# Performance work log

Hardware: AMD Instinct MI355X
Metric: run time of the kernel (lower is better)

The kernel has to match this reference:

```python
import jax, jax.numpy as jnp
import numpy as np

PATCH_W = 5  # from init_kwargs


def _fold(x, H, W, k):
    # x: (N, C*k*k, L) with L = (H-k+1)*(W-k+1), stride=1 col2im scatter-add
    N, CKK, L = x.shape
    oh, ow = H - k + 1, W - k + 1
    C = CKK // (k * k)
    x = x.reshape(N, C, k, k, oh, ow)
    out = jnp.zeros((N, C, H, W), x.dtype)
    for di in range(k):
        for dj in range(k):
            out = out.at[:, :, di:di + oh, dj:dj + ow].add(x[:, :, di, dj])
    return out


def _unfold(img, k):
    # img: (N, C, H, W) -> (N, C*k*k, L), stride=1 im2col gather
    N, C, H, W = img.shape
    oh, ow = H - k + 1, W - k + 1
    cols = jnp.stack(
        [img[:, :, di:di + oh, dj:dj + ow] for di in range(k) for dj in range(k)],
        axis=2,
    )  # (N, C, k*k, oh, ow)
    return cols.reshape(N, C * k * k, oh * ow)


def setup_inputs() -> dict:
    key = jax.random.key(0)
    images, hor_f, ver_f = 8, 64, 25
    pixels_h = pixels_w = 64
    patches = (pixels_h - PATCH_W + 1) * (pixels_w - PATCH_W + 1)  # 3600
    x = jax.random.normal(key, (images, patches, hor_f, ver_f), dtype=jnp.float32)
    return {"x": x, "pixels_h": pixels_h, "pixels_w": pixels_w}


def reference(x, pixels_h, pixels_w):
    k = PATCH_W
    images, patches, hor_f, ver_f = x.shape
    # (images, patches, hor_f, ver_f) -> (images*hor_f, ver_f, patches)
    xc = jnp.transpose(x, (0, 2, 3, 1)).reshape(images * hor_f, ver_f, patches)
    # overlap count per output pixel (fold of ones)
    ones = jnp.ones((1, ver_f, patches), xc.dtype)
    patch_cnt = _fold(ones, pixels_h, pixels_w, k)  # (1, C, H, W)
    img = _fold(xc, pixels_h, pixels_w, k) / patch_cnt
    cols = _unfold(img, k)  # (images*hor_f, ver_f, patches)
    out = cols.reshape(images, hor_f, ver_f, patches)
    return jnp.transpose(out, (0, 3, 1, 2))
```

## Files before the change

### kernel.cpp

```cpp
#include <hip/hip_runtime.h>

#define OH     60
#define NIMG   8
#define HF     64
#define VF     25
#define NPATCH 3600
#define CDIM   1600

typedef float floatx4 __attribute__((ext_vector_type(4)));

#define FH   8
#define FC   (FH * VF)
#define SPI  5
#define PJS  64
#define NSTRIP 12
#define SROWS  9

__global__ __launch_bounds__(512, 6) void fold_kernel(const float* __restrict__ x,
                                                      float* __restrict__ slab) {
    __shared__ float lb[FC * PJS];
    const int b = blockIdx.x;
    const int im = b & 7;
    const int rem = b >> 3;
    const int hg = rem & 7, strip = rem >> 3;
    const int t = threadIdx.x;
    const int h0 = hg * FH;
    const int pi0 = strip * SPI;
    const int j = t & 63, g = t >> 6;

    float acc[SROWS];
#pragma unroll
    for (int k = 0; k < SROWS; ++k) acc[k] = 0.f;

    const float* xb = x + ((size_t)im * NPATCH + (size_t)pi0 * OH) * CDIM + h0 * VF;

    int off_g[6], off_l[6];
#pragma unroll
    for (int k = 0; k < 6; ++k) {
        int u = t + 512 * k;
        if (u < 3000) {
            int pj = u / 50, c4 = u - 50 * pj;
            off_g[k] = pj * CDIM + (c4 << 2);
            off_l[k] = (c4 << 8) + (pj ^ (c4 & 31));
        }
    }

    float4 stg[6];
#pragma unroll
    for (int k = 0; k < 6; ++k)
        if (t + 512 * k < 3000)
            stg[k] = *reinterpret_cast<const float4*>(xb + off_g[k]);

#pragma unroll
    for (int row = 0; row < SPI; ++row) {
        if (row) __syncthreads();
#pragma unroll
        for (int k = 0; k < 6; ++k)
            if (t + 512 * k < 3000) {
                float4 v = stg[k];
                int a = off_l[k];
                lb[a]           = v.x;
                lb[a + PJS]     = v.y;
                lb[a + 2 * PJS] = v.z;
                lb[a + 3 * PJS] = v.w;
            }
        if (row + 1 < SPI) {
#pragma unroll
            for (int k = 0; k < 6; ++k)
                if (t + 512 * k < 3000)
                    stg[k] = *reinterpret_cast<const float4*>(
                        xb + (size_t)(row + 1) * OH * CDIM + off_g[k]);
        }
        __syncthreads();
#pragma unroll
        for (int di = 0; di < 5; ++di) {
#pragma unroll
            for (int dj = 0; dj < 5; ++dj) {
                int c = g * VF + di * 5 + dj;
                int pjr = j - dj;
                if ((unsigned)pjr < 60u)
                    acc[row + di] += lb[c * PJS + (pjr ^ ((c >> 2) & 31))];
            }
        }
    }

    float* sb = slab + (((size_t)(strip * 8 + im) * 64 + h0 + g) * SROWS) * 64 + j;
#pragma unroll
    for (int il = 0; il < SROWS; ++il) sb[il * 64] = acc[il];
}

#define UH   16
#define LJS  68

__global__ __launch_bounds__(256) void unfold_kernel(const float* __restrict__ slab,
                                                     float* __restrict__ out) {
    __shared__ float li[UH * 5 * LJS];
    __shared__ int4 lut[100];
    const int b = blockIdx.x;
    const int im = b & 7;
    const int rem = b >> 3;
    const int hh = rem & 3, pi = rem >> 2;
    const int t = threadIdx.x;
    const int h0 = hh * UH;

    if (t < 100) {
        int4 e;
        int* ep = &e.x;
#pragma unroll
        for (int k = 0; k < 4; ++k) {
            int fl = 4 * t + k;
            int ho = fl / 25, v = fl - 25 * ho;
            int di = v / 5, dj = v - 5 * di;
            ep[k] = (ho * 5 + di) * LJS + dj;
        }
        lut[t] = e;
    }

    for (int u = t; u < UH * 5 * 16; u += 256) {
        int ch = u / 80, rem2 = u - 80 * ch;
        int di = rem2 >> 4, j4 = rem2 & 15;
        int i = pi + di;
        int s_hi = min(i / 5, NSTRIP - 1);
        int s_lo = (i <= 8) ? 0 : (i - 4) / 5;
        const float* pa = slab +
            (((size_t)(s_lo * 8 + im) * 64 + h0 + ch) * SROWS + (i - 5 * s_lo)) * 64 + (j4 << 2);
        float4 v = *reinterpret_cast<const float4*>(pa);
        if (s_hi != s_lo) {
            const float* pb = slab +
                (((size_t)(s_hi * 8 + im) * 64 + h0 + ch) * SROWS + (i - 5 * s_hi)) * 64 + (j4 << 2);
            float4 w = *reinterpret_cast<const float4*>(pb);
            v.x += w.x; v.y += w.y; v.z += w.z; v.w += w.w;
        }
        float ri = 1.0f / (float)min(min(i + 1, 64 - i), 5);
        int jb = j4 << 2;
        float4 w;
        w.x = v.x * ri * (1.0f / (float)min(min(jb + 1, 64 - jb), 5));
        w.y = v.y * ri * (1.0f / (float)min(min(jb + 2, 63 - jb), 5));
        w.z = v.z * ri * (1.0f / (float)min(min(jb + 3, 62 - jb), 5));
        w.w = v.w * ri * (1.0f / (float)min(min(jb + 4, 61 - jb), 5));
        *reinterpret_cast<float4*>(&li[(ch * 5 + di) * LJS + jb]) = w;
    }
    __syncthreads();

    float* ob = out + ((size_t)im * NPATCH + (size_t)pi * OH) * CDIM + h0 * VF;
    for (int u = t; u < 6000; u += 256) {
        int pj = u / 100, r = u - 100 * pj;
        int4 e = lut[r];
        floatx4 o;
        o.x = li[e.x + pj];
        o.y = li[e.y + pj];
        o.z = li[e.z + pj];
        o.w = li[e.w + pj];
        __builtin_nontemporal_store(o,
            reinterpret_cast<floatx4*>(ob + (size_t)pj * CDIM + 4 * r));
    }
}

extern "C" void kernel_launch(void* const* d_in, const int* in_sizes, int n_in,
                              void* d_out, int out_size, void* d_ws, size_t ws_size,
                              hipStream_t stream) {
    const float* x = (const float*)d_in[0];
    float* slab = (float*)d_ws;
    float* out  = (float*)d_out;

    fold_kernel<<<768, 512, 0, stream>>>(x, slab);
    unfold_kernel<<<1920, 256, 0, stream>>>(slab, out);

    (void)out_size; (void)ws_size; (void)in_sizes; (void)n_in;
}
```

Before: 76.31 us.

## Fuse fold and unfold into one sliding-window kernel with halo recompute

```diff
diff --git a/kernel.cpp b/kernel.cpp
--- a/kernel.cpp
+++ b/kernel.cpp
@@ -9,30 +9,34 @@
 
 typedef float floatx4 __attribute__((ext_vector_type(4)));
 
-#define FH   8
-#define FC   (FH * VF)
-#define SPI  5
-#define PJS  64
-#define NSTRIP 12
-#define SROWS  9
+#define FH    8
+#define FC    200
+#define PJS   64
+#define SPP   15
+#define NACC  19
+#define JP2   65
+#define ROWSZ (8 * JP2)
 
-__global__ __launch_bounds__(512, 6) void fold_kernel(const float* __restrict__ x,
-                                                      float* __restrict__ slab) {
+__global__ __launch_bounds__(512) void fused_kernel(const float* __restrict__ x,
+                                                    float* __restrict__ out) {
     __shared__ float lb[FC * PJS];
+    __shared__ float li2[6 * ROWSZ];
     const int b = blockIdx.x;
     const int im = b & 7;
     const int rem = b >> 3;
     const int hg = rem & 7, strip = rem >> 3;
     const int t = threadIdx.x;
     const int h0 = hg * FH;
-    const int pi0 = strip * SPI;
+    const int pi0 = strip * SPP;
     const int j = t & 63, g = t >> 6;
 
-    float acc[SROWS];
+    const float rcj = 1.0f / (float)min(min(j + 1, 64 - j), 5);
+
+    float acc[NACC];
 #pragma unroll
-    for (int k = 0; k < SROWS; ++k) acc[k] = 0.f;
+    for (int k = 0; k < NACC; ++k) acc[k] = 0.f;
 
-    const float* xb = x + ((size_t)im * NPATCH + (size_t)pi0 * OH) * CDIM + h0 * VF;
+    const float* xb = x + (size_t)im * NPATCH * CDIM + h0 * VF;
 
     int off_g[6], off_l[6];
 #pragma unroll
@@ -45,114 +49,109 @@
         }
     }
 
+    int outoff[6], colb[6][4], dic[6][4];
+#pragma unroll
+    for (int k = 0; k < 6; ++k) {
+        int u = t + 512 * k;
+        if (u < 3000) {
+            int pj = u / 50, s = u - 50 * pj;
+            outoff[k] = pj * CDIM + (s << 2);
+#pragma unroll
+            for (int c = 0; c < 4; ++c) {
+                int fl = (s << 2) + c;
+                int ho = fl / 25, v = fl - 25 * ho;
+                int di = v / 5, dj = v - 5 * di;
+                colb[k][c] = ho * JP2 + pj + dj;
+                dic[k][c] = di;
+            }
+        }
+    }
+
     float4 stg[6];
-#pragma unroll
-    for (int k = 0; k < 6; ++k)
-        if (t + 512 * k < 3000)
-            stg[k] = *reinterpret_cast<const float4*>(xb + off_g[k]);
-
-#pragma unroll
-    for (int row = 0; row < SPI; ++row) {
-        if (row) __syncthreads();
-#pragma unroll
-        for (int k = 0; k < 6; ++k)
-            if (t + 512 * k < 3000) {
-                float4 v = stg[k];
-                int a = off_l[k];
-                lb[a]           = v.x;
-                lb[a + PJS]     = v.y;
-                lb[a + 2 * PJS] = v.z;
-                lb[a + 3 * PJS] = v.w;
-            }
-        if (row + 1 < SPI) {
+    {
+        int rho = pi0 - 4;
+        if (rho >= 0) {
 #pragma unroll
             for (int k = 0; k < 6; ++k)
                 if (t + 512 * k < 3000)
                     stg[k] = *reinterpret_cast<const float4*>(
-                        xb + (size_t)(row + 1) * OH * CDIM + off_g[k]);
-        }
-        __syncthreads();
-#pragma unroll
-        for (int di = 0; di < 5; ++di) {
-#pragma unroll
-            for (int dj = 0; dj < 5; ++dj) {
-                int c = g * VF + di * 5 + dj;
-                int pjr = j - dj;
-                if ((unsigned)pjr < 60u)
-                    acc[row + di] += lb[c * PJS + (pjr ^ ((c >> 2) & 31))];
-            }
+                        xb + (size_t)rho * OH * CDIM + off_g[k]);
         }
     }
 
-    float* sb = slab + (((size_t)(strip * 8 + im) * 64 + h0 + g) * SROWS) * 64 + j;
 #pragma unroll
-    for (int il = 0; il < SROWS; ++il) sb[il * 64] = acc[il];
-}
+    for (int r = 0; r < 24; ++r) {
+        const int rho = pi0 - 4 + r;
+        const bool sv = (r <= 22) && (rho >= 0) && (rho <= 59);
 
-#define UH   16
-#define LJS  68
+        if (sv) {
+#pragma unroll
+            for (int k = 0; k < 6; ++k)
+                if (t + 512 * k < 3000) {
+                    float4 v = stg[k];
+                    int a = off_l[k];
+                    lb[a]           = v.x;
+                    lb[a + PJS]     = v.y;
+                    lb[a + 2 * PJS] = v.z;
+                    lb[a + 3 * PJS] = v.w;
+                }
+        }
+        if (r >= 9) {
+            float* op = out + ((size_t)im * NPATCH + (size_t)(pi0 + r - 9) * OH) * CDIM
+                            + h0 * VF;
+            const int base = (r - 9) % 6;
+#pragma unroll
+            for (int k = 0; k < 6; ++k)
+                if (t + 512 * k < 3000) {
+                    floatx4 o;
+                    { int sl = base + dic[k][0]; sl -= (sl >= 6) ? 6 : 0;
+                      o.x = li2[sl * ROWSZ + colb[k][0]]; }
+                    { int sl = base + dic[k][1]; sl -= (sl >= 6) ? 6 : 0;
+                      o.y = li2[sl * ROWSZ + colb[k][1]]; }
+                    { int sl = base + dic[k][2]; sl -= (sl >= 6) ? 6 : 0;
+                      o.z = li2[sl * ROWSZ + colb[k][2]]; }
+                    { int sl = base + dic[k][3]; sl -= (sl >= 6) ? 6 : 0;
+                      o.w = li2[sl * ROWSZ + colb[k][3]]; }
+                    __builtin_nontemporal_store(o,
+                        reinterpret_cast<floatx4*>(op + outoff[k]));
+                }
+        }
+        __syncthreads();
 
-__global__ __launch_bounds__(256) void unfold_kernel(const float* __restrict__ slab,
-                                                     float* __restrict__ out) {
-    __shared__ float li[UH * 5 * LJS];
-    __shared__ int4 lut[100];
-    const int b = blockIdx.x;
-    const int im = b & 7;
-    const int rem = b >> 3;
-    const int hh = rem & 3, pi = rem >> 2;
-    const int t = threadIdx.x;
-    const int h0 = hh * UH;
-
-    if (t < 100) {
-        int4 e;
-        int* ep = &e.x;
+        if (sv) {
 #pragma unroll
-        for (int k = 0; k < 4; ++k) {
-            int fl = 4 * t + k;
-            int ho = fl / 25, v = fl - 25 * ho;
-            int di = v / 5, dj = v - 5 * di;
-            ep[k] = (ho * 5 + di) * LJS + dj;
+            for (int di = 0; di < 5; ++di) {
+                const int il = r - 4 + di;
+                if (il >= 0 && il < NACC) {
+#pragma unroll
+                    for (int dj = 0; dj < 5; ++dj) {
+                        int c = g * VF + di * 5 + dj;
+                        int pjr = j - dj;
+                        if ((unsigned)pjr < 60u)
+                            acc[il] += lb[c * PJS + (pjr ^ ((c >> 2) & 31))];
+                    }
+                }
+            }
         }
-        lut[t] = e;
-    }
-
-    for (int u = t; u < UH * 5 * 16; u += 256) {
-        int ch = u / 80, rem2 = u - 80 * ch;
-        int di = rem2 >> 4, j4 = rem2 & 15;
-        int i = pi + di;
-        int s_hi = min(i / 5, NSTRIP - 1);
-        int s_lo = (i <= 8) ? 0 : (i - 4) / 5;
-        const float* pa = slab +
-            (((size_t)(s_lo * 8 + im) * 64 + h0 + ch) * SROWS + (i - 5 * s_lo)) * 64 + (j4 << 2);
-        float4 v = *reinterpret_cast<const float4*>(pa);
-        if (s_hi != s_lo) {
-            const float* pb = slab +
-                (((size_t)(s_hi * 8 + im) * 64 + h0 + ch) * SROWS + (i - 5 * s_hi)) * 64 + (j4 << 2);
-            float4 w = *reinterpret_cast<const float4*>(pb);
-            v.x += w.x; v.y += w.y; v.z += w.z; v.w += w.w;
+        if (r < 23) {
+            int rho2 = rho + 1;
+            if (r + 1 <= 22 && rho2 >= 0 && rho2 <= 59) {
+#pragma unroll
+                for (int k = 0; k < 6; ++k)
+                    if (t + 512 * k < 3000)
+                        stg[k] = *reinterpret_cast<const float4*>(
+                            xb + (size_t)rho2 * OH * CDIM + off_g[k]);
+            }
         }
-        float ri = 1.0f / (float)min(min(i + 1, 64 - i), 5);
-        int jb = j4 << 2;
-        float4 w;
-        w.x = v.x * ri * (1.0f / (float)min(min(jb + 1, 64 - jb), 5));
-        w.y = v.y * ri * (1.0f / (float)min(min(jb + 2, 63 - jb), 5));
-        w.z = v.z * ri * (1.0f / (float)min(min(jb + 3, 62 - jb), 5));
-        w.w = v.w * ri * (1.0f / (float)min(min(jb + 4, 61 - jb), 5));
-        *reinterpret_cast<float4*>(&li[(ch * 5 + di) * LJS + jb]) = w;
-    }
-    __syncthreads();
-
-    float* ob = out + ((size_t)im * NPATCH + (size_t)pi * OH) * CDIM + h0 * VF;
-    for (int u = t; u < 6000; u += 256) {
-        int pj = u / 100, r = u - 100 * pj;
-        int4 e = lut[r];
-        floatx4 o;
-        o.x = li[e.x + pj];
-        o.y = li[e.y + pj];
-        o.z = li[e.z + pj];
-        o.w = li[e.w + pj];
-        __builtin_nontemporal_store(o,
-            reinterpret_cast<floatx4*>(ob + (size_t)pj * CDIM + 4 * r));
+        if (r >= 4 && r <= 22) {
+            const int il = r - 4;
+            const int i = pi0 + il;
+            float ri = 0.2f;
+            if (i < 4) ri = 1.0f / (float)(i + 1);
+            else if (i > 59) ri = 1.0f / (float)(64 - i);
+            li2[(il % 6) * ROWSZ + g * JP2 + j] = acc[il] * ri * rcj;
+        }
+        __syncthreads();
     }
 }
 
@@ -160,11 +159,9 @@
                               void* d_out, int out_size, void* d_ws, size_t ws_size,
                               hipStream_t stream) {
     const float* x = (const float*)d_in[0];
-    float* slab = (float*)d_ws;
-    float* out  = (float*)d_out;
+    float* out = (float*)d_out;
 
-    fold_kernel<<<768, 512, 0, stream>>>(x, slab);
-    unfold_kernel<<<1920, 256, 0, stream>>>(slab, out);
+    fused_kernel<<<256, 512, 0, stream>>>(x, out);
 
-    (void)out_size; (void)ws_size; (void)in_sizes; (void)n_in;
+    (void)out_size; (void)ws_size; (void)d_ws; (void)in_sizes; (void)n_in;
 }
```

Result: slower. 82.34 us (+7.9%).

## Make fold staging per-wave with scalar loads, removing block barriers

Applied to the files above, without the earlier changes.

```diff
diff --git a/kernel.cpp b/kernel.cpp
--- a/kernel.cpp
+++ b/kernel.cpp
@@ -10,15 +10,15 @@
 typedef float floatx4 __attribute__((ext_vector_type(4)));
 
 #define FH   8
-#define FC   (FH * VF)
 #define SPI  5
-#define PJS  64
 #define NSTRIP 12
 #define SROWS  9
+#define NF   1500
+#define WSTR 1536
 
 __global__ __launch_bounds__(512, 6) void fold_kernel(const float* __restrict__ x,
                                                       float* __restrict__ slab) {
-    __shared__ float lb[FC * PJS];
+    __shared__ float lb[FH * WSTR];
     const int b = blockIdx.x;
     const int im = b & 7;
     const int rem = b >> 3;
@@ -28,58 +28,40 @@
     const int pi0 = strip * SPI;
     const int j = t & 63, g = t >> 6;
 
+    float* lbw = lb + g * WSTR;
+
     float acc[SROWS];
 #pragma unroll
     for (int k = 0; k < SROWS; ++k) acc[k] = 0.f;
 
-    const float* xb = x + ((size_t)im * NPATCH + (size_t)pi0 * OH) * CDIM + h0 * VF;
+    const float* xb = x + ((size_t)im * NPATCH + (size_t)pi0 * OH) * CDIM
+                        + (h0 + g) * VF;
 
-    int off_g[6], off_l[6];
+    int off_g[24];
 #pragma unroll
-    for (int k = 0; k < 6; ++k) {
-        int u = t + 512 * k;
-        if (u < 3000) {
-            int pj = u / 50, c4 = u - 50 * pj;
-            off_g[k] = pj * CDIM + (c4 << 2);
-            off_l[k] = (c4 << 8) + (pj ^ (c4 & 31));
+    for (int s = 0; s < 24; ++s) {
+        int u = j + 64 * s;
+        if (u < NF) {
+            int pj = u / 25, v = u - 25 * pj;
+            off_g[s] = pj * CDIM + v;
         }
     }
 
-    float4 stg[6];
+    for (int row = 0; row < SPI; ++row) {
+        const float* xr = xb + (size_t)row * OH * CDIM;
 #pragma unroll
-    for (int k = 0; k < 6; ++k)
-        if (t + 512 * k < 3000)
-            stg[k] = *reinterpret_cast<const float4*>(xb + off_g[k]);
-
+        for (int s = 0; s < 24; ++s) {
+            int u = j + 64 * s;
+            if (u < NF) lbw[u] = xr[off_g[s]];
+        }
 #pragma unroll
-    for (int row = 0; row < SPI; ++row) {
-        if (row) __syncthreads();
+        for (int dj = 0; dj < 5; ++dj) {
+            int pjr = j - dj;
+            bool ok = (unsigned)pjr < 60u;
+            const float* pcol = lbw + pjr * 25;
 #pragma unroll
-        for (int k = 0; k < 6; ++k)
-            if (t + 512 * k < 3000) {
-                float4 v = stg[k];
-                int a = off_l[k];
-                lb[a]           = v.x;
-                lb[a + PJS]     = v.y;
-                lb[a + 2 * PJS] = v.z;
-                lb[a + 3 * PJS] = v.w;
-            }
-        if (row + 1 < SPI) {
-#pragma unroll
-            for (int k = 0; k < 6; ++k)
-                if (t + 512 * k < 3000)
-                    stg[k] = *reinterpret_cast<const float4*>(
-                        xb + (size_t)(row + 1) * OH * CDIM + off_g[k]);
-        }
-        __syncthreads();
-#pragma unroll
-        for (int di = 0; di < 5; ++di) {
-#pragma unroll
-            for (int dj = 0; dj < 5; ++dj) {
-                int c = g * VF + di * 5 + dj;
-                int pjr = j - dj;
-                if ((unsigned)pjr < 60u)
-                    acc[row + di] += lb[c * PJS + (pjr ^ ((c >> 2) & 31))];
+            for (int di = 0; di < 5; ++di) {
+                if (ok) acc[row + di] += pcol[di * 5 + dj];
             }
         }
     }
```

Measured after the change: 77.83 us. Within noise of the previous version (+2.0%).
